# Optimization experiments

Hardware: AMD Instinct MI355X
Metric: run time of the kernel (lower is better)

Reference implementation:

```python
import jax, jax.numpy as jnp
import numpy as np

DIM = 1024
NUM_HEADS = 16
HEAD_DIM = DIM // NUM_HEADS
SCALE = HEAD_DIM ** -0.5
B, N = 4, 2048


def setup_inputs() -> dict:
    key = jax.random.key(0)
    ks = jax.random.split(key, 5)
    s = 1.0 / np.sqrt(DIM)  # ~ torch Linear init scale
    x = jax.random.normal(ks[0], (B, N, DIM), dtype=jnp.float32)
    Wq = jax.random.normal(ks[1], (DIM, DIM), dtype=jnp.float32) * s
    Wk = jax.random.normal(ks[2], (DIM, DIM), dtype=jnp.float32) * s
    Wv = jax.random.normal(ks[3], (DIM, DIM), dtype=jnp.float32) * s
    Wo = jax.random.normal(ks[4], (DIM, DIM), dtype=jnp.float32) * s
    mask = jnp.tril(jnp.ones((N, N), dtype=bool))  # causal 2D bool mask
    return {"x": x, "mask": mask, "Wq": Wq, "Wk": Wk, "Wv": Wv, "Wo": Wo}


def reference(x, mask, Wq, Wk, Wv, Wo):
    Bb, Nn, D = x.shape
    def split_heads(t):
        return t.reshape(Bb, Nn, NUM_HEADS, HEAD_DIM).transpose(0, 2, 1, 3)  # [B,H,N,d]
    q = split_heads(x @ Wq.T)
    k = split_heads(x @ Wk.T)
    v = split_heads(x @ Wv.T)
    attn = jnp.einsum('bhqd,bhkd->bhqk', q, k) * SCALE  # [B,H,N,N]
    # 2D mask -> broadcast over batch and heads; ~mask positions set to -inf
    attn = jnp.where(mask[None, None, :, :], attn, -jnp.inf)
    attn = jax.nn.softmax(attn, axis=-1)
    out = jnp.einsum('bhqk,bhkd->bhqd', attn, v)
    out = out.transpose(0, 2, 1, 3).reshape(Bb, Nn, D)
    return out @ Wo.T
```

## Files before the change

### kernel.cpp

```cpp
#include <hip/hip_runtime.h>
#include <stdint.h>

#define Bq   4
#define Nseq 2048
#define NH   16
#define HD   64
#define DIMD 1024

typedef float  f32x4  __attribute__((ext_vector_type(4)));
typedef __bf16 bf16x8 __attribute__((ext_vector_type(8)));
typedef short  s16x4  __attribute__((ext_vector_type(4)));

typedef __attribute__((address_space(1))) void as1_void;
typedef __attribute__((address_space(3))) void as3_void;

static __device__ __forceinline__ uint16_t f2bf(float f) {
    uint32_t u = __builtin_bit_cast(uint32_t, f);
    u += 0x7fffu + ((u >> 16) & 1u);
    return (uint16_t)(u >> 16);
}

static __device__ __forceinline__ uint32_t pk2(float a, float b) {
    uint32_t ua = __builtin_bit_cast(uint32_t, a);
    uint32_t ub = __builtin_bit_cast(uint32_t, b);
    return (ua >> 16) | (ub & 0xffff0000u);
}

static __device__ __forceinline__ void asyncLoad16(const uint16_t* g, uint16_t* l) {
    __builtin_amdgcn_global_load_lds((as1_void*)g, (as3_void*)l, 16, 0, 0);
}

static __device__ __forceinline__ void storeOut(float* p, float v)    { *p = v; }
static __device__ __forceinline__ void storeOut(uint16_t* p, float v) { *p = f2bf(v); }

__global__ void cast_all(const float* __restrict__ x,
                         const float* __restrict__ wq, const float* __restrict__ wk,
                         const float* __restrict__ wv, const float* __restrict__ wo,
                         uint16_t* __restrict__ dst) {
    size_t i = ((size_t)blockIdx.x * blockDim.x + threadIdx.x) * 4;
    const float* src; size_t off; float scale = 1.0f;
    if (i < 8388608) { src = x; off = i; }
    else {
        size_t wI = i - 8388608;
        size_t wi = wI >> 20;
        off = wI & 1048575;
        src = (wi == 0) ? wq : (wi == 1) ? wk : (wi == 2) ? wv : wo;
        if (wi == 0) scale = 0.18033688011112042f;
    }
    float4 v = *(const float4*)(src + off);
    ushort4 o;
    o.x = f2bf(v.x * scale); o.y = f2bf(v.y * scale);
    o.z = f2bf(v.z * scale); o.w = f2bf(v.w * scale);
    *(ushort4*)(dst + i) = o;
}

template <typename OutT>
__global__ __launch_bounds__(256) void gemm_bt(
    const uint16_t* __restrict__ A, const uint16_t* __restrict__ W0,
    OutT* __restrict__ C0, int K, int Nld, int blocksPerSec,
    size_t wSecStride, size_t cSecStride, uint16_t* __restrict__ vtb, int vSec)
{
    __shared__ __align__(16) uint16_t As[128*32];
    __shared__ __align__(16) uint16_t Bs[128*32];

    const int t = threadIdx.x, lane = t & 63, w = t >> 6;
    const int wr = w >> 1, wc = w & 1;

    const int sec = blockIdx.x / blocksPerSec;
    const int n0  = (blockIdx.x % blocksPerSec) * 128;
    const int m0  = blockIdx.y * 128;
    const uint16_t* Wp = W0 + (size_t)sec * wSecStride;
    OutT* C = C0 + (size_t)sec * cSecStride;

    const int s0 = t, s1 = t + 256;
    const int r0 = s0 >> 2, g0 = (s0 & 3) ^ (r0 & 3);
    const int r1 = s1 >> 2, g1 = (s1 & 3) ^ (r1 & 3);
    uint16_t* ldsA0 = As + (size_t)(w*64) * 8;
    uint16_t* ldsA1 = As + (size_t)(256 + w*64) * 8;
    uint16_t* ldsB0 = Bs + (size_t)(w*64) * 8;
    uint16_t* ldsB1 = Bs + (size_t)(256 + w*64) * 8;

    int aoff[4], boff[4];
    {
        const int c = lane >> 4;
        #pragma unroll
        for (int i = 0; i < 4; ++i) {
            int m = wr*64 + i*16 + (lane & 15);
            aoff[i] = (m*4 + (c ^ (m & 3))) * 8;
            int n = wc*64 + i*16 + (lane & 15);
            boff[i] = (n*4 + (c ^ (n & 3))) * 8;
        }
    }

    f32x4 acc[4][4] = {};

    for (int k0 = 0; k0 < K; k0 += 32) {
        __syncthreads();
        asyncLoad16(A  + (size_t)(m0 + r0)*K + k0 + g0*8, ldsA0);
        asyncLoad16(A  + (size_t)(m0 + r1)*K + k0 + g1*8, ldsA1);
        asyncLoad16(Wp + (size_t)(n0 + r0)*K + k0 + g0*8, ldsB0);
        asyncLoad16(Wp + (size_t)(n0 + r1)*K + k0 + g1*8, ldsB1);
        __syncthreads();

        bf16x8 af[4], bfr[4];
        #pragma unroll
        for (int i = 0; i < 4; ++i) af[i]  = *(const bf16x8*)(As + aoff[i]);
        #pragma unroll
        for (int i = 0; i < 4; ++i) bfr[i] = *(const bf16x8*)(Bs + boff[i]);
        #pragma unroll
        for (int mt = 0; mt < 4; ++mt)
            #pragma unroll
            for (int nt = 0; nt < 4; ++nt)
                acc[mt][nt] = __builtin_amdgcn_mfma_f32_16x16x32_bf16(
                    af[mt], bfr[nt], acc[mt][nt], 0, 0, 0);
    }

    if (vtb != nullptr && sec == vSec) {
        #pragma unroll
        for (int mt = 0; mt < 4; ++mt)
            #pragma unroll
            for (int nt = 0; nt < 4; ++nt) {
                int rowg = m0 + wr*64 + mt*16 + ((lane >> 4) << 2);
                int colg = n0 + wc*64 + nt*16 + (lane & 15);
                int bb = rowg >> 11, nn = rowg & 2047;
                int hh = colg >> 6,  dd = colg & 63;
                ushort4 o4;
                o4.x = f2bf(acc[mt][nt][0]); o4.y = f2bf(acc[mt][nt][1]);
                o4.z = f2bf(acc[mt][nt][2]); o4.w = f2bf(acc[mt][nt][3]);
                *(ushort4*)(vtb + ((size_t)((bb*NH + hh)*HD + dd))*Nseq + nn) = o4;
            }
    } else {
        #pragma unroll
        for (int mt = 0; mt < 4; ++mt)
            #pragma unroll
            for (int nt = 0; nt < 4; ++nt)
                #pragma unroll
                for (int r = 0; r < 4; ++r) {
                    int row = m0 + wr*64 + mt*16 + ((lane >> 4) << 2) + r;
                    int col = n0 + wc*64 + nt*16 + (lane & 15);
                    storeOut(&C[(size_t)row * Nld + col], acc[mt][nt][r]);
                }
    }
}

__global__ __launch_bounds__(256, 3) void attn(
    const uint16_t* __restrict__ Q, const uint16_t* __restrict__ K,
    const uint16_t* __restrict__ Vt, uint16_t* __restrict__ O)
{
    __shared__ __align__(16) uint16_t Qs[128*64];
    __shared__ __align__(16) uint16_t Kb[2][64*64];
    __shared__ __align__(16) uint16_t Vb[2][64*64];

    const int t = threadIdx.x, lane = t & 63, w = t >> 6;
    const int quad = lane >> 4, c = lane & 15;
    const int pair = blockIdx.x;
    const int bh = blockIdx.y, b = bh >> 4, h = bh & 15;
    const size_t tokBase = (size_t)b * Nseq;
    const int hcol = h * HD;

    #define STAGE_Q(q0_)                                                     \
        _Pragma("unroll")                                                    \
        for (int i = 0; i < 4; ++i) {                                        \
            int s = t + 256*i;                                               \
            int row = s >> 3, gg = (s & 7) ^ (row & 7);                      \
            asyncLoad16(Q + (tokBase + (q0_) + row)*DIMD + hcol + gg*8,      \
                        Qs + (size_t)(w*64 + 256*i)*8);                      \
        }

    #define STAGE_KV(k0_, buf_)                                             \
        _Pragma("unroll")                                                    \
        for (int i = 0; i < 2; ++i) {                                        \
            int s = t + 256*i;                                               \
            int row = s >> 3, gg = (s & 7) ^ (row & 7);                      \
            asyncLoad16(K + (tokBase + (k0_) + row)*DIMD + hcol + gg*8,      \
                        Kb[buf_] + (size_t)(w*64 + 256*i)*8);                \
            asyncLoad16(Vt + ((size_t)bh*HD + row)*Nseq + (k0_) + gg*8,      \
                        Vb[buf_] + (size_t)(w*64 + 256*i)*8);                \
        }

    STAGE_Q(pair*128);
    STAGE_KV(0, 0);

    int g = 0;
    for (int sp = 0; sp < 2; ++sp) {
        const int qi = sp ? (15 - pair) : pair;
        const int q0 = qi * 128;
        const int wrow0 = q0 + w*32;
        const int end = 2*qi + 2;

        bf16x8 qf[2][2];
        f32x4  o[2][4] = {};
        float  l_lane[2] = {0.f, 0.f};

        for (int kt = 0; kt < end; ++kt, ++g) {
            const int cur = g & 1, nxt = cur ^ 1;
            const int k0 = kt * 64;
            __syncthreads();

            if (kt == 0) {
                #pragma unroll
                for (int qt = 0; qt < 2; ++qt)
                    #pragma unroll
                    for (int ks = 0; ks < 2; ++ks) {
                        int row = w*32 + qt*16 + c;
                        int pos = (ks*4 + quad) ^ (row & 7);
                        qf[qt][ks] = *(const bf16x8*)(Qs + (size_t)(row*8 + pos)*8);
                    }
            }

            if (kt + 1 < end)      { STAGE_KV((kt+1)*64, nxt); }
            else if (sp == 0)      { STAGE_KV(0, nxt); }
            if (sp == 0 && kt == 1) { STAGE_Q((15-pair)*128); }

            if (k0 > wrow0 + 31) continue;

            const uint16_t* Ks = Kb[cur];
            const uint16_t* Vs = Vb[cur];

            f32x4 sv[2][4] = {};
            #pragma unroll
            for (int nt = 0; nt < 4; ++nt)
                #pragma unroll
                for (int ks = 0; ks < 2; ++ks) {
                    int row = nt*16 + c;
                    int pos = (ks*4 + quad) ^ (row & 7);
                    bf16x8 kf = *(const bf16x8*)(Ks + (size_t)(row*8 + pos)*8);
                    sv[0][nt] = __builtin_amdgcn_mfma_f32_16x16x32_bf16(kf, qf[0][ks], sv[0][nt], 0, 0, 0);
                    sv[1][nt] = __builtin_amdgcn_mfma_f32_16x16x32_bf16(kf, qf[1][ks], sv[1][nt], 0, 0, 0);
                }

            if (k0 + 63 > wrow0) {
                #pragma unroll
                for (int qt = 0; qt < 2; ++qt)
                    #pragma unroll
                    for (int nt = 0; nt < 4; ++nt)
                        #pragma unroll
                        for (int r = 0; r < 4; ++r) {
                            int kvg = k0 + nt*16 + quad*4 + r;
                            int qg  = wrow0 + qt*16 + c;
                            if (kvg > qg) sv[qt][nt][r] = -340.0f;
                        }
            }

            s16x4 pb[2][4];
            #pragma unroll
            for (int qt = 0; qt < 2; ++qt)
                #pragma unroll
                for (int nt = 0; nt < 4; ++nt) {
                    float p0 = __builtin_amdgcn_exp2f(sv[qt][nt][0]);
                    float p1 = __builtin_amdgcn_exp2f(sv[qt][nt][1]);
                    float p2 = __builtin_amdgcn_exp2f(sv[qt][nt][2]);
                    float p3 = __builtin_amdgcn_exp2f(sv[qt][nt][3]);
                    l_lane[qt] += (p0 + p1) + (p2 + p3);
                    union { uint32_t u[2]; s16x4 v; } pu;
                    pu.u[0] = pk2(p0, p1);
                    pu.u[1] = pk2(p2, p3);
                    pb[qt][nt] = pu.v;
                }

            #pragma unroll
            for (int s4 = 0; s4 < 4; ++s4)
                #pragma unroll
                for (int dt = 0; dt < 4; ++dt) {
                    int row = dt*16 + c;
                    int chunk = s4*2 + (quad >> 1);
                    int pos = chunk ^ (row & 7);
                    s16x4 vf = *(const s16x4*)(Vs + (size_t)(row*8 + pos)*8 + (quad & 1)*4);
                    o[0][dt] = __builtin_amdgcn_mfma_f32_16x16x16bf16_1k(vf, pb[0][s4], o[0][dt], 0, 0, 0);
                    o[1][dt] = __builtin_amdgcn_mfma_f32_16x16x16bf16_1k(vf, pb[1][s4], o[1][dt], 0, 0, 0);
                }
        }

        #pragma unroll
        for (int qt = 0; qt < 2; ++qt) {
            float l = l_lane[qt];
            l += __shfl_xor(l, 16);
            l += __shfl_xor(l, 32);
            float inv = 1.0f / l;
            int tok = (int)(q0 + w*32 + qt*16 + c);
            #pragma unroll
            for (int dt = 0; dt < 4; ++dt) {
                ushort4 o4;
                o4.x = f2bf(o[qt][dt][0] * inv);
                o4.y = f2bf(o[qt][dt][1] * inv);
                o4.z = f2bf(o[qt][dt][2] * inv);
                o4.w = f2bf(o[qt][dt][3] * inv);
                *(ushort4*)(O + (tokBase + tok)*DIMD + hcol + dt*16 + quad*4) = o4;
            }
        }
    }
    #undef STAGE_Q
    #undef STAGE_KV
}

extern "C" void kernel_launch(void* const* d_in, const int* in_sizes, int n_in,
                              void* d_out, int out_size, void* d_ws, size_t ws_size,
                              hipStream_t stream) {
    const float* x  = (const float*)d_in[0];
    const float* Wq = (const float*)d_in[2];
    const float* Wk = (const float*)d_in[3];
    const float* Wv = (const float*)d_in[4];
    const float* Wo = (const float*)d_in[5];

    uint16_t* ws  = (uint16_t*)d_ws;
    uint16_t* xb  = ws;
    uint16_t* wqb = ws + 8388608;
    uint16_t* wob = wqb + 3*1048576;
    uint16_t* qb  = ws + 12582912;
    uint16_t* kb  = qb + 8388608;
    uint16_t* vtb = kb + 8388608;
    uint16_t* ab  = xb;

    cast_all<<<12288, 256, 0, stream>>>(x, Wq, Wk, Wv, Wo, ws);

    gemm_bt<uint16_t><<<dim3(24, 64), 256, 0, stream>>>(
        xb, wqb, qb, DIMD, DIMD, 8, (size_t)1048576, (size_t)8388608, vtb, 2);

    attn<<<dim3(8, 64), 256, 0, stream>>>(qb, kb, vtb, ab);

    gemm_bt<float><<<dim3(8, 64), 256, 0, stream>>>(
        ab, wob, (float*)d_out, DIMD, DIMD, 8, (size_t)0, (size_t)0, nullptr, -1);
}
```

Measured before the change: 279.4 us.

## Split paired causal attention blocks into one q-tile per block; change GEMM LDS swizzle

The attention kernel now launches one workgroup per 128-row query tile instead of pairing tile i with tile 15-i. Heavy tiles are ordered first. The Q staging buffer aliases the K buffer, which shrinks LDS use and allows occupancy to rise from 3 to 4 blocks per CU. Separately, the GEMM LDS XOR swizzle now keys on row>>1 to reduce bank conflicts. The trade-off is that per-block load balance now relies on the hardware scheduler and no longer on pairing, and the block count doubles.

```diff
diff --git a/kernel.cpp b/kernel.cpp
--- a/kernel.cpp
+++ b/kernel.cpp
@@ -73,8 +73,8 @@
     OutT* C = C0 + (size_t)sec * cSecStride;
 
     const int s0 = t, s1 = t + 256;
-    const int r0 = s0 >> 2, g0 = (s0 & 3) ^ (r0 & 3);
-    const int r1 = s1 >> 2, g1 = (s1 & 3) ^ (r1 & 3);
+    const int r0 = s0 >> 2, g0 = (s0 & 3) ^ ((r0 >> 1) & 3);
+    const int r1 = s1 >> 2, g1 = (s1 & 3) ^ ((r1 >> 1) & 3);
     uint16_t* ldsA0 = As + (size_t)(w*64) * 8;
     uint16_t* ldsA1 = As + (size_t)(256 + w*64) * 8;
     uint16_t* ldsB0 = Bs + (size_t)(w*64) * 8;
@@ -86,9 +86,9 @@
         #pragma unroll
         for (int i = 0; i < 4; ++i) {
             int m = wr*64 + i*16 + (lane & 15);
-            aoff[i] = (m*4 + (c ^ (m & 3))) * 8;
+            aoff[i] = (m*4 + (c ^ ((m >> 1) & 3))) * 8;
             int n = wc*64 + i*16 + (lane & 15);
-            boff[i] = (n*4 + (c ^ (n & 3))) * 8;
+            boff[i] = (n*4 + (c ^ ((n >> 1) & 3))) * 8;
         }
     }
 
@@ -143,29 +143,22 @@
     }
 }
 
-__global__ __launch_bounds__(256, 3) void attn(
+__global__ __launch_bounds__(256, 4) void attn(
     const uint16_t* __restrict__ Q, const uint16_t* __restrict__ K,
     const uint16_t* __restrict__ Vt, uint16_t* __restrict__ O)
 {
-    __shared__ __align__(16) uint16_t Qs[128*64];
     __shared__ __align__(16) uint16_t Kb[2][64*64];
     __shared__ __align__(16) uint16_t Vb[2][64*64];
 
     const int t = threadIdx.x, lane = t & 63, w = t >> 6;
     const int quad = lane >> 4, c = lane & 15;
-    const int pair = blockIdx.x;
+    const int x = blockIdx.x;
+    const int qi = (x < 8) ? (15 - x) : (x - 8);
+    const int q0 = qi * 128;
     const int bh = blockIdx.y, b = bh >> 4, h = bh & 15;
     const size_t tokBase = (size_t)b * Nseq;
     const int hcol = h * HD;
-
-    #define STAGE_Q(q0_)                                                     \
-        _Pragma("unroll")                                                    \
-        for (int i = 0; i < 4; ++i) {                                        \
-            int s = t + 256*i;                                               \
-            int row = s >> 3, gg = (s & 7) ^ (row & 7);                      \
-            asyncLoad16(Q + (tokBase + (q0_) + row)*DIMD + hcol + gg*8,      \
-                        Qs + (size_t)(w*64 + 256*i)*8);                      \
-        }
+    uint16_t* Qs = (uint16_t*)Kb;
 
     #define STAGE_KV(k0_, buf_)                                             \
         _Pragma("unroll")                                                    \
@@ -178,118 +171,114 @@
                         Vb[buf_] + (size_t)(w*64 + 256*i)*8);                \
         }
 
-    STAGE_Q(pair*128);
+    #pragma unroll
+    for (int i = 0; i < 4; ++i) {
+        int s = t + 256*i;
+        int row = s >> 3, gg = (s & 7) ^ (row & 7);
+        asyncLoad16(Q + (tokBase + q0 + row)*DIMD + hcol + gg*8,
+                    Qs + (size_t)(w*64 + 256*i)*8);
+    }
+    __syncthreads();
+    bf16x8 qf[2][2];
+    #pragma unroll
+    for (int qt = 0; qt < 2; ++qt)
+        #pragma unroll
+        for (int ks = 0; ks < 2; ++ks) {
+            int row = w*32 + qt*16 + c;
+            int pos = (ks*4 + quad) ^ (row & 7);
+            qf[qt][ks] = *(const bf16x8*)(Qs + (size_t)(row*8 + pos)*8);
+        }
+    __syncthreads();
     STAGE_KV(0, 0);
 
-    int g = 0;
-    for (int sp = 0; sp < 2; ++sp) {
-        const int qi = sp ? (15 - pair) : pair;
-        const int q0 = qi * 128;
-        const int wrow0 = q0 + w*32;
-        const int end = 2*qi + 2;
-
-        bf16x8 qf[2][2];
-        f32x4  o[2][4] = {};
-        float  l_lane[2] = {0.f, 0.f};
-
-        for (int kt = 0; kt < end; ++kt, ++g) {
-            const int cur = g & 1, nxt = cur ^ 1;
-            const int k0 = kt * 64;
-            __syncthreads();
-
-            if (kt == 0) {
-                #pragma unroll
-                for (int qt = 0; qt < 2; ++qt)
-                    #pragma unroll
-                    for (int ks = 0; ks < 2; ++ks) {
-                        int row = w*32 + qt*16 + c;
-                        int pos = (ks*4 + quad) ^ (row & 7);
-                        qf[qt][ks] = *(const bf16x8*)(Qs + (size_t)(row*8 + pos)*8);
-                    }
+    const int wrow0 = q0 + w*32;
+    const int end = 2*qi + 2;
+    f32x4  o[2][4] = {};
+    float  l_lane[2] = {0.f, 0.f};
+
+    for (int kt = 0; kt < end; ++kt) {
+        const int cur = kt & 1, nxt = cur ^ 1;
+        const int k0 = kt * 64;
+        __syncthreads();
+
+        if (kt + 1 < end) { STAGE_KV((kt+1)*64, nxt); }
+
+        if (k0 > wrow0 + 31) continue;
+
+        const uint16_t* Ks = Kb[cur];
+        const uint16_t* Vs = Vb[cur];
+
+        f32x4 sv[2][4] = {};
+        #pragma unroll
+        for (int nt = 0; nt < 4; ++nt)
+            #pragma unroll
+            for (int ks = 0; ks < 2; ++ks) {
+                int row = nt*16 + c;
+                int pos = (ks*4 + quad) ^ (row & 7);
+                bf16x8 kf = *(const bf16x8*)(Ks + (size_t)(row*8 + pos)*8);
+                sv[0][nt] = __builtin_amdgcn_mfma_f32_16x16x32_bf16(kf, qf[0][ks], sv[0][nt], 0, 0, 0);
+                sv[1][nt] = __builtin_amdgcn_mfma_f32_16x16x32_bf16(kf, qf[1][ks], sv[1][nt], 0, 0, 0);
             }
 
-            if (kt + 1 < end)      { STAGE_KV((kt+1)*64, nxt); }
-            else if (sp == 0)      { STAGE_KV(0, nxt); }
-            if (sp == 0 && kt == 1) { STAGE_Q((15-pair)*128); }
-
-            if (k0 > wrow0 + 31) continue;
-
-            const uint16_t* Ks = Kb[cur];
-            const uint16_t* Vs = Vb[cur];
-
-            f32x4 sv[2][4] = {};
-            #pragma unroll
-            for (int nt = 0; nt < 4; ++nt)
-                #pragma unroll
-                for (int ks = 0; ks < 2; ++ks) {
-                    int row = nt*16 + c;
-                    int pos = (ks*4 + quad) ^ (row & 7);
-                    bf16x8 kf = *(const bf16x8*)(Ks + (size_t)(row*8 + pos)*8);
-                    sv[0][nt] = __builtin_amdgcn_mfma_f32_16x16x32_bf16(kf, qf[0][ks], sv[0][nt], 0, 0, 0);
-                    sv[1][nt] = __builtin_amdgcn_mfma_f32_16x16x32_bf16(kf, qf[1][ks], sv[1][nt], 0, 0, 0);
-                }
-
-            if (k0 + 63 > wrow0) {
-                #pragma unroll
-                for (int qt = 0; qt < 2; ++qt)
-                    #pragma unroll
-                    for (int nt = 0; nt < 4; ++nt)
-                        #pragma unroll
-                        for (int r = 0; r < 4; ++r) {
-                            int kvg = k0 + nt*16 + quad*4 + r;
-                            int qg  = wrow0 + qt*16 + c;
-                            if (kvg > qg) sv[qt][nt][r] = -340.0f;
-                        }
-            }
-
-            s16x4 pb[2][4];
+        if (k0 + 63 > wrow0) {
             #pragma unroll
             for (int qt = 0; qt < 2; ++qt)
                 #pragma unroll
-                for (int nt = 0; nt < 4; ++nt) {
-                    float p0 = __builtin_amdgcn_exp2f(sv[qt][nt][0]);
-                    float p1 = __builtin_amdgcn_exp2f(sv[qt][nt][1]);
-                    float p2 = __builtin_amdgcn_exp2f(sv[qt][nt][2]);
-                    float p3 = __builtin_amdgcn_exp2f(sv[qt][nt][3]);
-                    l_lane[qt] += (p0 + p1) + (p2 + p3);
-                    union { uint32_t u[2]; s16x4 v; } pu;
-                    pu.u[0] = pk2(p0, p1);
-                    pu.u[1] = pk2(p2, p3);
-                    pb[qt][nt] = pu.v;
-                }
-
-            #pragma unroll
-            for (int s4 = 0; s4 < 4; ++s4)
-                #pragma unroll
-                for (int dt = 0; dt < 4; ++dt) {
-                    int row = dt*16 + c;
-                    int chunk = s4*2 + (quad >> 1);
-                    int pos = chunk ^ (row & 7);
-                    s16x4 vf = *(const s16x4*)(Vs + (size_t)(row*8 + pos)*8 + (quad & 1)*4);
-                    o[0][dt] = __builtin_amdgcn_mfma_f32_16x16x16bf16_1k(vf, pb[0][s4], o[0][dt], 0, 0, 0);
-                    o[1][dt] = __builtin_amdgcn_mfma_f32_16x16x16bf16_1k(vf, pb[1][s4], o[1][dt], 0, 0, 0);
-                }
-        }
-
-        #pragma unroll
-        for (int qt = 0; qt < 2; ++qt) {
-            float l = l_lane[qt];
-            l += __shfl_xor(l, 16);
-            l += __shfl_xor(l, 32);
-            float inv = 1.0f / l;
-            int tok = (int)(q0 + w*32 + qt*16 + c);
+                for (int nt = 0; nt < 4; ++nt)
+                    #pragma unroll
+                    for (int r = 0; r < 4; ++r) {
+                        int kvg = k0 + nt*16 + quad*4 + r;
+                        int qg  = wrow0 + qt*16 + c;
+                        if (kvg > qg) sv[qt][nt][r] = -340.0f;
+                    }
+        }
+
+        s16x4 pb[2][4];
+        #pragma unroll
+        for (int qt = 0; qt < 2; ++qt)
+            #pragma unroll
+            for (int nt = 0; nt < 4; ++nt) {
+                float p0 = __builtin_amdgcn_exp2f(sv[qt][nt][0]);
+                float p1 = __builtin_amdgcn_exp2f(sv[qt][nt][1]);
+                float p2 = __builtin_amdgcn_exp2f(sv[qt][nt][2]);
+                float p3 = __builtin_amdgcn_exp2f(sv[qt][nt][3]);
+                l_lane[qt] += (p0 + p1) + (p2 + p3);
+                union { uint32_t u[2]; s16x4 v; } pu;
+                pu.u[0] = pk2(p0, p1);
+                pu.u[1] = pk2(p2, p3);
+                pb[qt][nt] = pu.v;
+            }
+
+        #pragma unroll
+        for (int s4 = 0; s4 < 4; ++s4)
             #pragma unroll
             for (int dt = 0; dt < 4; ++dt) {
-                ushort4 o4;
-                o4.x = f2bf(o[qt][dt][0] * inv);
-                o4.y = f2bf(o[qt][dt][1] * inv);
-                o4.z = f2bf(o[qt][dt][2] * inv);
-                o4.w = f2bf(o[qt][dt][3] * inv);
-                *(ushort4*)(O + (tokBase + tok)*DIMD + hcol + dt*16 + quad*4) = o4;
+                int row = dt*16 + c;
+                int chunk = s4*2 + (quad >> 1);
+                int pos = chunk ^ (row & 7);
+                s16x4 vf = *(const s16x4*)(Vs + (size_t)(row*8 + pos)*8 + (quad & 1)*4);
+                o[0][dt] = __builtin_amdgcn_mfma_f32_16x16x16bf16_1k(vf, pb[0][s4], o[0][dt], 0, 0, 0);
+                o[1][dt] = __builtin_amdgcn_mfma_f32_16x16x16bf16_1k(vf, pb[1][s4], o[1][dt], 0, 0, 0);
             }
-        }
-    }
-    #undef STAGE_Q
+    }
+
+    #pragma unroll
+    for (int qt = 0; qt < 2; ++qt) {
+        float l = l_lane[qt];
+        l += __shfl_xor(l, 16);
+        l += __shfl_xor(l, 32);
+        float inv = 1.0f / l;
+        int tok = (int)(q0 + w*32 + qt*16 + c);
+        #pragma unroll
+        for (int dt = 0; dt < 4; ++dt) {
+            ushort4 o4;
+            o4.x = f2bf(o[qt][dt][0] * inv);
+            o4.y = f2bf(o[qt][dt][1] * inv);
+            o4.z = f2bf(o[qt][dt][2] * inv);
+            o4.w = f2bf(o[qt][dt][3] * inv);
+            *(ushort4*)(O + (tokBase + tok)*DIMD + hcol + dt*16 + quad*4) = o4;
+        }
+    }
     #undef STAGE_KV
 }
 
@@ -316,7 +305,7 @@
     gemm_bt<uint16_t><<<dim3(24, 64), 256, 0, stream>>>(
         xb, wqb, qb, DIMD, DIMD, 8, (size_t)1048576, (size_t)8388608, vtb, 2);
 
-    attn<<<dim3(8, 64), 256, 0, stream>>>(qb, kb, vtb, ab);
+    attn<<<dim3(16, 64), 256, 0, stream>>>(qb, kb, vtb, ab);
 
     gemm_bt<float><<<dim3(8, 64), 256, 0, stream>>>(
         ab, wob, (float*)d_out, DIMD, DIMD, 8, (size_t)0, (size_t)0, nullptr, -1);
```

After: 295.6 us. +5.8%, slower.
